# Kernel tuning notes

Hardware: AMD Instinct MI355X
Metric: run time of the kernel (lower is better)

The kernel has to match this reference:

```python
import jax, jax.numpy as jnp
import numpy as np

DIM = 512
HEADS = 8
DIM_HEAD = 64
INNER = HEADS * DIM_HEAD  # 512
SCALE = DIM_HEAD ** -0.5


def setup_inputs() -> dict:
    key = jax.random.key(0)
    k1, k2, k3, k4 = jax.random.split(key, 4)
    x = jax.random.normal(k1, (4, 2048, DIM), dtype=jnp.float32)
    # Dense(inner_dim*3, use_bias=False): weight [dim, 3*inner]
    w_qkv = jax.random.normal(k2, (DIM, 3 * INNER), dtype=jnp.float32) * (DIM ** -0.5)
    # to_out Dense(dim): weight [inner, dim] + bias [dim]
    w_out = jax.random.normal(k3, (INNER, DIM), dtype=jnp.float32) * (INNER ** -0.5)
    b_out = jax.random.normal(k4, (DIM,), dtype=jnp.float32) * 0.01
    return {"x": x, "w_qkv": w_qkv, "w_out": w_out, "b_out": b_out}


def reference(x, w_qkv, w_out, b_out):
    b, n, _ = x.shape
    qkv = x @ w_qkv                                  # [b, n, 3*inner]
    q, k, v = jnp.split(qkv, 3, axis=-1)             # each [b, n, inner]
    def to_heads(t):
        return t.reshape(b, n, HEADS, DIM_HEAD).transpose(0, 2, 1, 3)  # [b, h, n, d]
    q, k, v = map(to_heads, (q, k, v))
    dots = jnp.einsum('bhid,bhjd->bhij', q, k) * SCALE
    attn = jax.nn.softmax(dots, axis=-1)
    out = jnp.einsum('bhij,bhjd->bhid', attn, v)     # [b, h, n, d]
    out = out.transpose(0, 2, 1, 3).reshape(b, n, INNER)
    return out @ w_out + b_out                       # [b, n, dim]
```

## Files before the change

### kernel.cpp

```cpp
#include <hip/hip_runtime.h>
#include <stdint.h>

#define DIM    512
#define HEADS  8
#define DHEAD  64
#define SEQ    2048
#define BATCH  4
#define BH     (BATCH*HEADS)
#define MROWS  (BATCH*SEQ)
#define NQKV   (3*DIM)
#define QSCALE 0.18033688011112042f

typedef __bf16 bf16x8 __attribute__((ext_vector_type(8)));
typedef float  f32x4  __attribute__((ext_vector_type(4)));

typedef unsigned short u16;

#if __has_builtin(__builtin_amdgcn_exp2f)
#define EXP2(x) __builtin_amdgcn_exp2f(x)
#else
#define EXP2(x) exp2f(x)
#endif

__device__ __forceinline__ u16 f2bf(float f) {
    union { float f; uint32_t u; } v; v.f = f;
    uint32_t u = v.u;
    uint32_t r = (u + 0x7FFFu + ((u >> 16) & 1u)) >> 16;
    return (u16)r;
}
__device__ __forceinline__ float bf2f(u16 h) {
    union { uint32_t u; float f; } v; v.u = ((uint32_t)h) << 16;
    return v.f;
}
__device__ __forceinline__ uint32_t pk2bf(float a, float b) {
    union { float f; uint32_t u; } ua, ub; ua.f = a; ub.f = b;
#if __has_builtin(__builtin_amdgcn_perm)
    return __builtin_amdgcn_perm(ub.u + 0x8000u, ua.u + 0x8000u, 0x07060302u);
#else
    return ((ua.u + 0x8000u) >> 16) | ((ub.u + 0x8000u) & 0xFFFF0000u);
#endif
}

__device__ __forceinline__ void async16(const void* g, u16* l) {
    __builtin_amdgcn_global_load_lds(
        (const __attribute__((address_space(1))) void*)g,
        (__attribute__((address_space(3))) void*)l, 16, 0, 0);
}

__global__ void detect_dtype(const u16* __restrict__ x, int* __restrict__ flag) {
    __shared__ int cnt;
    if (threadIdx.x == 0) cnt = 0;
    __syncthreads();
    u16 v = x[threadIdx.x * 2];
    int e = (v >> 7) & 0xFF;
    int ok = (v == 0) || (e >= 100 && e <= 140);
    atomicAdd(&cnt, ok);
    __syncthreads();
    if (threadIdx.x == 0) *flag = (cnt >= 192) ? 1 : 0;
}

__global__ void pack_x(const void* __restrict__ xin, const int* __restrict__ flag,
                       u16* __restrict__ xb) {
    int i = blockIdx.x * 256 + threadIdx.x;
    int isbf = *flag;
    if (isbf) {
        ((uint2*)xb)[i] = ((const uint2*)xin)[i];
    } else {
        float4 v = ((const float4*)xin)[i];
        ushort4 o;
        o.x = f2bf(v.x); o.y = f2bf(v.y); o.z = f2bf(v.z); o.w = f2bf(v.w);
        ((ushort4*)xb)[i] = o;
    }
}

__global__ void pack_wt(const void* __restrict__ win, const int* __restrict__ flag,
                        u16* __restrict__ wt, int K, int N) {
    int idx = blockIdx.x * 256 + threadIdx.x;
    if (idx >= K * N) return;
    int k = idx / N, n = idx - k * N;
    int isbf = *flag;
    u16 v = isbf ? ((const u16*)win)[idx] : f2bf(((const float*)win)[idx]);
    wt[(size_t)n * K + k] = v;
}

template<int KDIM, int TM, int TN>
__device__ __forceinline__ void gemm_lds(
        const u16* __restrict__ A, const u16* __restrict__ Bt,
        int m0, int n0, int tid, u16* As, u16* Bs,
        f32x4 (&acc)[TM / 32][TN / 32]) {
    int lane = tid & 63, ln = lane & 15, quad = lane >> 4, w = tid >> 6;
    int wm = (w >> 1) * (TM / 2), wn = (w & 1) * (TN / 2);

    auto stage = [&](int k0) {
#pragma unroll
        for (int ii = 0; ii < TM / 64; ++ii) {
            int r0 = (ii * 4 + w) * 16;
            int row = r0 + (lane >> 2);
            int seg = (lane & 3) ^ (row & 3);
            async16(A + (size_t)(m0 + row) * KDIM + k0 + seg * 8, As + r0 * 32);
        }
#pragma unroll
        for (int ii = 0; ii < TN / 64; ++ii) {
            int r0 = (ii * 4 + w) * 16;
            int row = r0 + (lane >> 2);
            int seg = (lane & 3) ^ (row & 3);
            async16(Bt + (size_t)(n0 + row) * KDIM + k0 + seg * 8, Bs + r0 * 32);
        }
    };

    stage(0);
#pragma unroll 1
    for (int kk = 0; kk < KDIM / 32; ++kk) {
        __syncthreads();
        bf16x8 a[TM / 32], b[TN / 32];
        int rseg = (quad ^ (ln & 3)) * 8;
#pragma unroll
        for (int i = 0; i < TM / 32; ++i)
            a[i] = *(const bf16x8*)(As + (wm + i * 16 + ln) * 32 + rseg);
#pragma unroll
        for (int j = 0; j < TN / 32; ++j)
            b[j] = *(const bf16x8*)(Bs + (wn + j * 16 + ln) * 32 + rseg);
#pragma unroll
        for (int i = 0; i < TM / 32; ++i)
#pragma unroll
            for (int j = 0; j < TN / 32; ++j)
                acc[i][j] = __builtin_amdgcn_mfma_f32_16x16x32_bf16(
                    a[i], b[j], acc[i][j], 0, 0, 0);
        __syncthreads();
        if (kk + 1 < KDIM / 32) stage((kk + 1) * 32);
    }
}

__global__ __launch_bounds__(256, 3) void qkv_gemm(
        const u16* __restrict__ X, const u16* __restrict__ Wt,
        u16* __restrict__ Qb, u16* __restrict__ Kb, u16* __restrict__ Vt) {
    __shared__ __align__(16) u16 As[128 * 32];
    __shared__ __align__(16) u16 Bs[128 * 32];

    int tid  = threadIdx.x;
    int lane = tid & 63, ln = lane & 15, quad = lane >> 4, wid = tid >> 6;
    int m0 = blockIdx.x * 128, n0 = blockIdx.y * 128;
    int wm = (wid >> 1) * 64, wn = (wid & 1) * 64;

    f32x4 acc[4][4];
#pragma unroll
    for (int i = 0; i < 4; ++i)
#pragma unroll
        for (int j = 0; j < 4; ++j) acc[i][j] = 0.f;

    gemm_lds<DIM, 128, 128>(X, Wt, m0, n0, tid, As, Bs, acc);

#pragma unroll
    for (int j = 0; j < 4; ++j) {
        int col   = n0 + wn + j * 16 + ln;
        int which = col >> 9;
        int hd    = col & 511;
        int h     = hd >> 6, d = hd & 63;
#pragma unroll
        for (int i = 0; i < 4; ++i) {
            int rbase = m0 + wm + i * 16 + quad * 4;
            if (which == 2) {
                int b = rbase >> 11, n = rbase & 2047;
                int bh = b * HEADS + h;
                uint2 pv;
                pv.x = pk2bf(acc[i][j][0], acc[i][j][1]);
                pv.y = pk2bf(acc[i][j][2], acc[i][j][3]);
                *(uint2*)&Vt[((size_t)bh * DHEAD + d) * SEQ + n] = pv;
            } else {
#pragma unroll
                for (int r = 0; r < 4; ++r) {
                    int row = rbase + r;
                    int b = row >> 11, n = row & 2047;
                    int bh = b * HEADS + h;
                    if (which == 0)
                        Qb[((size_t)bh * SEQ + n) * DHEAD + d] = f2bf(acc[i][j][r] * QSCALE);
                    else
                        Kb[((size_t)bh * SEQ + n) * DHEAD + d] = f2bf(acc[i][j][r]);
                }
            }
        }
    }
}

#define PSTRIDE 80
__global__ __launch_bounds__(256, 2) void flash_attn(
        const u16* __restrict__ Qb, const u16* __restrict__ Kb,
        const u16* __restrict__ Vt, u16* __restrict__ Ob) {
    __shared__ __align__(16) u16 Kc[2][64 * 64];
    __shared__ __align__(16) u16 Vc[2][64 * 64];
    __shared__ __align__(16) u16 Pl[4][32 * PSTRIDE];

    int tid  = threadIdx.x;
    int lane = tid & 63, ln = lane & 15, quad = lane >> 4, wid = tid >> 6;
    int bh = blockIdx.x;
    int q0 = blockIdx.y * 128 + wid * 32;

    const u16* Qh = Qb + (size_t)bh * SEQ * DHEAD;
    const u16* Kh = Kb + (size_t)bh * SEQ * DHEAD;
    const u16* Vh = Vt + (size_t)bh * DHEAD * SEQ;

    int srow = lane >> 3;
    int gseg = (lane & 7) ^ srow;

    auto stageKV = [&](int buf, int kc) {
#pragma unroll
        for (int ii = 0; ii < 2; ++ii) {
            int slab = wid + ii * 4;
            const u16* gk = Kh + (size_t)(kc + slab * 8 + srow) * DHEAD + gseg * 8;
            async16(gk, &Kc[buf][slab * 8 * 64]);
            const u16* gv = Vh + (size_t)(slab * 8 + srow) * SEQ + kc + gseg * 8;
            async16(gv, &Vc[buf][slab * 8 * 64]);
        }
    };

    bf16x8 qf[2][2];
#pragma unroll
    for (int qt = 0; qt < 2; ++qt)
#pragma unroll
        for (int s = 0; s < 2; ++s)
            qf[qt][s] = *(const bf16x8*)(
                Qh + (size_t)(q0 + qt * 16 + ln) * DHEAD + s * 32 + quad * 8);

    f32x4 o[2][4];
#pragma unroll
    for (int qt = 0; qt < 2; ++qt)
#pragma unroll
        for (int t = 0; t < 4; ++t) o[qt][t] = 0.f;
    float lsum[2] = {0.f, 0.f};

    stageKV(0, 0);
    __syncthreads();

#pragma unroll 1
    for (int kc = 0; kc < SEQ; kc += 64) {
        int cur = (kc >> 6) & 1;
        if (kc + 64 < SEQ) stageKV(cur ^ 1, kc + 64);

        bf16x8 kf[4][2], vf[4][2];
#pragma unroll
        for (int kt = 0; kt < 4; ++kt) {
            int row = kt * 16 + ln;
#pragma unroll
            for (int s = 0; s < 2; ++s) {
                int seg = (s * 4 + quad) ^ (ln & 7);
                kf[kt][s] = *(const bf16x8*)&Kc[cur][row * 64 + seg * 8];
                vf[kt][s] = *(const bf16x8*)&Vc[cur][row * 64 + seg * 8];
            }
        }

        f32x4 st[4][2];
#pragma unroll
        for (int kt = 0; kt < 4; ++kt)
#pragma unroll
            for (int qt = 0; qt < 2; ++qt) st[kt][qt] = 0.f;
#pragma unroll
        for (int kt = 0; kt < 4; ++kt)
#pragma unroll
            for (int qt = 0; qt < 2; ++qt)
#pragma unroll
                for (int s = 0; s < 2; ++s)
                    st[kt][qt] = __builtin_amdgcn_mfma_f32_16x16x32_bf16(
                        kf[kt][s], qf[qt][s], st[kt][qt], 0, 0, 0);

#pragma unroll
        for (int qt = 0; qt < 2; ++qt)
#pragma unroll
            for (int kt = 0; kt < 4; ++kt) {
                float p0 = EXP2(st[kt][qt][0]);
                float p1 = EXP2(st[kt][qt][1]);
                float p2 = EXP2(st[kt][qt][2]);
                float p3 = EXP2(st[kt][qt][3]);
                lsum[qt] += (p0 + p1) + (p2 + p3);
                uint2 d;
                d.x = pk2bf(p0, p1);
                d.y = pk2bf(p2, p3);
                *(uint2*)&Pl[wid][(qt * 16 + ln) * PSTRIDE + kt * 16 + quad * 4] = d;
            }

        bf16x8 pf[2][2];
#pragma unroll
        for (int qt = 0; qt < 2; ++qt)
#pragma unroll
            for (int s = 0; s < 2; ++s)
                pf[qt][s] = *(const bf16x8*)
                    &Pl[wid][(qt * 16 + ln) * PSTRIDE + s * 32 + quad * 8];

#pragma unroll
        for (int t = 0; t < 4; ++t)
#pragma unroll
            for (int s = 0; s < 2; ++s)
#pragma unroll
                for (int qt = 0; qt < 2; ++qt)
                    o[qt][t] = __builtin_amdgcn_mfma_f32_16x16x32_bf16(
                        pf[qt][s], vf[t][s], o[qt][t], 0, 0, 0);

        __syncthreads();
    }

#pragma unroll
    for (int qt = 0; qt < 2; ++qt) {
        float s = lsum[qt];
        s += __shfl_xor(s, 16);
        s += __shfl_xor(s, 32);
        lsum[qt] = 1.0f / s;
    }

    int b = bh >> 3, h = bh & 7;
#pragma unroll
    for (int qt = 0; qt < 2; ++qt) {
#pragma unroll
        for (int t = 0; t < 4; ++t) {
            int d = t * 16 + ln;
#pragma unroll
            for (int r = 0; r < 4; ++r) {
                int qrow = quad * 4 + r;
                float inv = __shfl(lsum[qt], qrow);
                int n = q0 + qt * 16 + qrow;
                Ob[((size_t)(b * SEQ + n)) * DIM + h * DHEAD + d] =
                    f2bf(o[qt][t][r] * inv);
            }
        }
    }
}

__global__ __launch_bounds__(256, 3) void out_gemm(
        const u16* __restrict__ A, const u16* __restrict__ Wt,
        const void* __restrict__ bias, void* __restrict__ out,
        const int* __restrict__ flag) {
    __shared__ __align__(16) u16 As[64 * 32];
    __shared__ __align__(16) u16 Bs[128 * 32];

    int tid  = threadIdx.x;
    int lane = tid & 63, ln = lane & 15, quad = lane >> 4, wid = tid >> 6;
    int m0 = blockIdx.x * 64, n0 = blockIdx.y * 128;
    int wm = (wid >> 1) * 32, wn = (wid & 1) * 64;
    int isbf = *flag;

    f32x4 acc[2][4];
#pragma unroll
    for (int i = 0; i < 2; ++i)
#pragma unroll
        for (int j = 0; j < 4; ++j) acc[i][j] = 0.f;

    gemm_lds<DIM, 64, 128>(A, Wt, m0, n0, tid, As, Bs, acc);

#pragma unroll
    for (int j = 0; j < 4; ++j) {
        int col = n0 + wn + j * 16 + ln;
        float bv = isbf ? bf2f(((const u16*)bias)[col])
                        : ((const float*)bias)[col];
#pragma unroll
        for (int i = 0; i < 2; ++i) {
            int rbase = m0 + wm + i * 16 + quad * 4;
#pragma unroll
            for (int r = 0; r < 4; ++r) {
                int row = rbase + r;
                size_t off = (size_t)row * DIM + col;
                float val = acc[i][j][r] + bv;
                if (isbf) ((u16*)out)[off] = f2bf(val);
                else      ((float*)out)[off] = val;
            }
        }
    }
}

extern "C" void kernel_launch(void* const* d_in, const int* in_sizes, int n_in,
                              void* d_out, int out_size, void* d_ws, size_t ws_size,
                              hipStream_t stream) {
    const void* x     = d_in[0];
    const void* w_qkv = d_in[1];
    const void* w_out = d_in[2];
    const void* b_out = d_in[3];

    int* flag   = (int*)d_ws;
    u16* x_bf   = (u16*)((char*)d_ws + 16);
    u16* wt_qkv = x_bf + (size_t)MROWS * DIM;
    u16* wt_out = wt_qkv + (size_t)NQKV * DIM;
    u16* Qb     = wt_out + (size_t)DIM * DIM;
    u16* Kb     = Qb + (size_t)BH * SEQ * DHEAD;
    u16* Vt     = Kb + (size_t)BH * SEQ * DHEAD;
    u16* attn   = x_bf;

    detect_dtype<<<1, 256, 0, stream>>>((const u16*)x, flag);
    pack_x<<<(MROWS * DIM / 4) / 256, 256, 0, stream>>>(x, flag, x_bf);
    pack_wt<<<(DIM * NQKV + 255) / 256, 256, 0, stream>>>(w_qkv, flag, wt_qkv, DIM, NQKV);
    pack_wt<<<(DIM * DIM + 255) / 256, 256, 0, stream>>>(w_out, flag, wt_out, DIM, DIM);
    qkv_gemm<<<dim3(MROWS / 128, NQKV / 128), 256, 0, stream>>>(x_bf, wt_qkv, Qb, Kb, Vt);
    flash_attn<<<dim3(BH, SEQ / 128), 256, 0, stream>>>(Qb, Kb, Vt, attn);
    out_gemm<<<dim3(MROWS / 64, DIM / 128), 256, 0, stream>>>(attn, wt_out, b_out, d_out, flag);
}
```

Measured before the change: 182.3 us.

## Fuse prep kernels, double-buffer GEMM LDS, swizzle P tile, shrink out_gemm tile

Merges dtype detection and the x and weight packing kernels into one launch, with each block recomputing the dtype flag itself. Both GEMMs now double-buffer their LDS tiles so the next K-slice load is issued before the current MFMAs, which drops one barrier per iteration. The attention P scratch tile switches from padded rows to an XOR-swizzled layout to cut LDS footprint while avoiding bank conflicts. out_gemm uses 64x64 tiles with more blocks per CU for better occupancy, at the cost of more LDS per GEMM block and less reuse per tile.

```diff
diff --git a/kernel.cpp b/kernel.cpp
--- a/kernel.cpp
+++ b/kernel.cpp
@@ -47,95 +47,106 @@
         (__attribute__((address_space(3))) void*)l, 16, 0, 0);
 }
 
-__global__ void detect_dtype(const u16* __restrict__ x, int* __restrict__ flag) {
+#define XBLKS  (MROWS * DIM / 4 / 256)
+#define WQBLKS (DIM * NQKV / 256)
+#define WOBLKS (DIM * DIM / 256)
+__global__ void prep(const void* __restrict__ x, const void* __restrict__ wq,
+                     const void* __restrict__ wo, u16* __restrict__ xb,
+                     u16* __restrict__ wtq, u16* __restrict__ wto,
+                     int* __restrict__ flag) {
     __shared__ int cnt;
-    if (threadIdx.x == 0) cnt = 0;
+    int tid = threadIdx.x;
+    if (tid == 0) cnt = 0;
     __syncthreads();
-    u16 v = x[threadIdx.x * 2];
-    int e = (v >> 7) & 0xFF;
-    int ok = (v == 0) || (e >= 100 && e <= 140);
-    atomicAdd(&cnt, ok);
+    {
+        u16 v = ((const u16*)x)[tid * 2];
+        int e = (v >> 7) & 0xFF;
+        atomicAdd(&cnt, (v == 0) || (e >= 100 && e <= 140));
+    }
     __syncthreads();
-    if (threadIdx.x == 0) *flag = (cnt >= 192) ? 1 : 0;
-}
-
-__global__ void pack_x(const void* __restrict__ xin, const int* __restrict__ flag,
-                       u16* __restrict__ xb) {
-    int i = blockIdx.x * 256 + threadIdx.x;
-    int isbf = *flag;
-    if (isbf) {
-        ((uint2*)xb)[i] = ((const uint2*)xin)[i];
+    int isbf = (cnt >= 192);
+    int b = blockIdx.x;
+    if (b == 0 && tid == 0) *flag = isbf;
+
+    if (b < XBLKS) {
+        int i = b * 256 + tid;
+        if (isbf) {
+            ((uint2*)xb)[i] = ((const uint2*)x)[i];
+        } else {
+            float4 v = ((const float4*)x)[i];
+            ushort4 o;
+            o.x = f2bf(v.x); o.y = f2bf(v.y); o.z = f2bf(v.z); o.w = f2bf(v.w);
+            ((ushort4*)xb)[i] = o;
+        }
+    } else if (b < XBLKS + WQBLKS) {
+        int idx = (b - XBLKS) * 256 + tid;
+        int k = idx / NQKV, n = idx - k * NQKV;
+        u16 v = isbf ? ((const u16*)wq)[idx] : f2bf(((const float*)wq)[idx]);
+        wtq[(size_t)n * DIM + k] = v;
     } else {
-        float4 v = ((const float4*)xin)[i];
-        ushort4 o;
-        o.x = f2bf(v.x); o.y = f2bf(v.y); o.z = f2bf(v.z); o.w = f2bf(v.w);
-        ((ushort4*)xb)[i] = o;
-    }
-}
-
-__global__ void pack_wt(const void* __restrict__ win, const int* __restrict__ flag,
-                        u16* __restrict__ wt, int K, int N) {
-    int idx = blockIdx.x * 256 + threadIdx.x;
-    if (idx >= K * N) return;
-    int k = idx / N, n = idx - k * N;
-    int isbf = *flag;
-    u16 v = isbf ? ((const u16*)win)[idx] : f2bf(((const float*)win)[idx]);
-    wt[(size_t)n * K + k] = v;
+        int idx = (b - XBLKS - WQBLKS) * 256 + tid;
+        int k = idx >> 9, n = idx & 511;
+        u16 v = isbf ? ((const u16*)wo)[idx] : f2bf(((const float*)wo)[idx]);
+        wto[(size_t)n * DIM + k] = v;
+    }
 }
 
 template<int KDIM, int TM, int TN>
-__device__ __forceinline__ void gemm_lds(
+__device__ __forceinline__ void gemm_lds_db(
         const u16* __restrict__ A, const u16* __restrict__ Bt,
         int m0, int n0, int tid, u16* As, u16* Bs,
         f32x4 (&acc)[TM / 32][TN / 32]) {
     int lane = tid & 63, ln = lane & 15, quad = lane >> 4, w = tid >> 6;
     int wm = (w >> 1) * (TM / 2), wn = (w & 1) * (TN / 2);
 
-    auto stage = [&](int k0) {
+    auto stage = [&](int buf, int k0) {
 #pragma unroll
         for (int ii = 0; ii < TM / 64; ++ii) {
             int r0 = (ii * 4 + w) * 16;
             int row = r0 + (lane >> 2);
             int seg = (lane & 3) ^ (row & 3);
-            async16(A + (size_t)(m0 + row) * KDIM + k0 + seg * 8, As + r0 * 32);
+            async16(A + (size_t)(m0 + row) * KDIM + k0 + seg * 8,
+                    As + buf * TM * 32 + r0 * 32);
         }
 #pragma unroll
         for (int ii = 0; ii < TN / 64; ++ii) {
             int r0 = (ii * 4 + w) * 16;
             int row = r0 + (lane >> 2);
             int seg = (lane & 3) ^ (row & 3);
-            async16(Bt + (size_t)(n0 + row) * KDIM + k0 + seg * 8, Bs + r0 * 32);
+            async16(Bt + (size_t)(n0 + row) * KDIM + k0 + seg * 8,
+                    Bs + buf * TN * 32 + r0 * 32);
         }
     };
 
-    stage(0);
+    stage(0, 0);
 #pragma unroll 1
     for (int kk = 0; kk < KDIM / 32; ++kk) {
         __syncthreads();
+        if (kk + 1 < KDIM / 32) stage((kk + 1) & 1, (kk + 1) * 32);
+        const u16* Ac = As + (kk & 1) * TM * 32;
+        const u16* Bc = Bs + (kk & 1) * TN * 32;
         bf16x8 a[TM / 32], b[TN / 32];
         int rseg = (quad ^ (ln & 3)) * 8;
 #pragma unroll
         for (int i = 0; i < TM / 32; ++i)
-            a[i] = *(const bf16x8*)(As + (wm + i * 16 + ln) * 32 + rseg);
+            a[i] = *(const bf16x8*)(Ac + (wm + i * 16 + ln) * 32 + rseg);
 #pragma unroll
         for (int j = 0; j < TN / 32; ++j)
-            b[j] = *(const bf16x8*)(Bs + (wn + j * 16 + ln) * 32 + rseg);
+            b[j] = *(const bf16x8*)(Bc + (wn + j * 16 + ln) * 32 + rseg);
 #pragma unroll
         for (int i = 0; i < TM / 32; ++i)
 #pragma unroll
             for (int j = 0; j < TN / 32; ++j)
                 acc[i][j] = __builtin_amdgcn_mfma_f32_16x16x32_bf16(
                     a[i], b[j], acc[i][j], 0, 0, 0);
-        __syncthreads();
-        if (kk + 1 < KDIM / 32) stage((kk + 1) * 32);
     }
 }
 
 __global__ __launch_bounds__(256, 3) void qkv_gemm(
         const u16* __restrict__ X, const u16* __restrict__ Wt,
         u16* __restrict__ Qb, u16* __restrict__ Kb, u16* __restrict__ Vt) {
-    __shared__ __align__(16) u16 As[128 * 32];
-    __shared__ __align__(16) u16 Bs[128 * 32];
+    __shared__ __align__(16) u16 As[2 * 128 * 32];
+    __shared__ __align__(16) u16 Bs[2 * 128 * 32];
 
     int tid  = threadIdx.x;
     int lane = tid & 63, ln = lane & 15, quad = lane >> 4, wid = tid >> 6;
@@ -148,7 +159,7 @@
 #pragma unroll
         for (int j = 0; j < 4; ++j) acc[i][j] = 0.f;
 
-    gemm_lds<DIM, 128, 128>(X, Wt, m0, n0, tid, As, Bs, acc);
+    gemm_lds_db<DIM, 128, 128>(X, Wt, m0, n0, tid, As, Bs, acc);
 
 #pragma unroll
     for (int j = 0; j < 4; ++j) {
@@ -182,13 +193,12 @@
     }
 }
 
-#define PSTRIDE 80
 __global__ __launch_bounds__(256, 2) void flash_attn(
         const u16* __restrict__ Qb, const u16* __restrict__ Kb,
         const u16* __restrict__ Vt, u16* __restrict__ Ob) {
     __shared__ __align__(16) u16 Kc[2][64 * 64];
     __shared__ __align__(16) u16 Vc[2][64 * 64];
-    __shared__ __align__(16) u16 Pl[4][32 * PSTRIDE];
+    __shared__ __align__(16) u16 Pl[4][32 * 64];
 
     int tid  = threadIdx.x;
     int lane = tid & 63, ln = lane & 15, quad = lane >> 4, wid = tid >> 6;
@@ -274,16 +284,18 @@
                 uint2 d;
                 d.x = pk2bf(p0, p1);
                 d.y = pk2bf(p2, p3);
-                *(uint2*)&Pl[wid][(qt * 16 + ln) * PSTRIDE + kt * 16 + quad * 4] = d;
+                int seg = (kt * 2 + (quad >> 1)) ^ (ln & 7);
+                *(uint2*)&Pl[wid][(qt * 16 + ln) * 64 + seg * 8 + (quad & 1) * 4] = d;
             }
 
         bf16x8 pf[2][2];
 #pragma unroll
         for (int qt = 0; qt < 2; ++qt)
 #pragma unroll
-            for (int s = 0; s < 2; ++s)
-                pf[qt][s] = *(const bf16x8*)
-                    &Pl[wid][(qt * 16 + ln) * PSTRIDE + s * 32 + quad * 8];
+            for (int s = 0; s < 2; ++s) {
+                int seg = (s * 4 + quad) ^ (ln & 7);
+                pf[qt][s] = *(const bf16x8*)&Pl[wid][(qt * 16 + ln) * 64 + seg * 8];
+            }
 
 #pragma unroll
         for (int t = 0; t < 4; ++t)
@@ -323,29 +335,29 @@
     }
 }
 
-__global__ __launch_bounds__(256, 3) void out_gemm(
+__global__ __launch_bounds__(256, 4) void out_gemm(
         const u16* __restrict__ A, const u16* __restrict__ Wt,
         const void* __restrict__ bias, void* __restrict__ out,
         const int* __restrict__ flag) {
-    __shared__ __align__(16) u16 As[64 * 32];
-    __shared__ __align__(16) u16 Bs[128 * 32];
+    __shared__ __align__(16) u16 As[2 * 64 * 32];
+    __shared__ __align__(16) u16 Bs[2 * 64 * 32];
 
     int tid  = threadIdx.x;
     int lane = tid & 63, ln = lane & 15, quad = lane >> 4, wid = tid >> 6;
-    int m0 = blockIdx.x * 64, n0 = blockIdx.y * 128;
-    int wm = (wid >> 1) * 32, wn = (wid & 1) * 64;
+    int m0 = blockIdx.x * 64, n0 = blockIdx.y * 64;
+    int wm = (wid >> 1) * 32, wn = (wid & 1) * 32;
     int isbf = *flag;
 
-    f32x4 acc[2][4];
+    f32x4 acc[2][2];
 #pragma unroll
     for (int i = 0; i < 2; ++i)
 #pragma unroll
-        for (int j = 0; j < 4; ++j) acc[i][j] = 0.f;
-
-    gemm_lds<DIM, 64, 128>(A, Wt, m0, n0, tid, As, Bs, acc);
-
-#pragma unroll
-    for (int j = 0; j < 4; ++j) {
+        for (int j = 0; j < 2; ++j) acc[i][j] = 0.f;
+
+    gemm_lds_db<DIM, 64, 64>(A, Wt, m0, n0, tid, As, Bs, acc);
+
+#pragma unroll
+    for (int j = 0; j < 2; ++j) {
         int col = n0 + wn + j * 16 + ln;
         float bv = isbf ? bf2f(((const u16*)bias)[col])
                         : ((const float*)bias)[col];
@@ -381,11 +393,9 @@
     u16* Vt     = Kb + (size_t)BH * SEQ * DHEAD;
     u16* attn   = x_bf;
 
-    detect_dtype<<<1, 256, 0, stream>>>((const u16*)x, flag);
-    pack_x<<<(MROWS * DIM / 4) / 256, 256, 0, stream>>>(x, flag, x_bf);
-    pack_wt<<<(DIM * NQKV + 255) / 256, 256, 0, stream>>>(w_qkv, flag, wt_qkv, DIM, NQKV);
-    pack_wt<<<(DIM * DIM + 255) / 256, 256, 0, stream>>>(w_out, flag, wt_out, DIM, DIM);
+    prep<<<XBLKS + WQBLKS + WOBLKS, 256, 0, stream>>>(
+        x, w_qkv, w_out, x_bf, wt_qkv, wt_out, flag);
     qkv_gemm<<<dim3(MROWS / 128, NQKV / 128), 256, 0, stream>>>(x_bf, wt_qkv, Qb, Kb, Vt);
     flash_attn<<<dim3(BH, SEQ / 128), 256, 0, stream>>>(Qb, Kb, Vt, attn);
-    out_gemm<<<dim3(MROWS / 64, DIM / 128), 256, 0, stream>>>(attn, wt_out, b_out, d_out, flag);
-}
+    out_gemm<<<dim3(MROWS / 64, DIM / 64), 256, 0, stream>>>(attn, wt_out, b_out, d_out, flag);
+}
```

After: 178.3 us. 2.2% less time.
